# Kernel tuning notes

Measured on AMD Instinct MI355X. Metric: run time of the kernel, lower is better.

Reference implementation:

```python
import jax, jax.numpy as jnp
import numpy as np

W_RAD = 2  # box-filter radius (init kwarg w)
KSIZE = 2 * W_RAD + 1


def _box_conv3d(x, kernel):
    # x: [B,1,D,H,W], kernel: [1,1,k,k,k]; 'same' padding, stride 1
    return jax.lax.conv_general_dilated(
        x, kernel,
        window_strides=(1, 1, 1),
        padding=[(W_RAD, W_RAD)] * 3,
        dimension_numbers=("NCDHW", "OIDHW", "NCDHW"),
    )


def setup_inputs() -> dict:
    key = jax.random.key(0)
    k1, k2 = jax.random.split(key)
    shape = (2, 1, 160, 160, 160)
    M = jax.random.uniform(k1, shape, dtype=jnp.float32)
    R = jax.random.uniform(k2, shape, dtype=jnp.float32)
    kernel = jnp.ones((1, 1, KSIZE, KSIZE, KSIZE), dtype=jnp.float32) / (KSIZE ** 3)
    return {"M": M, "R": R, "kernel": kernel}


def reference(M, R, kernel):
    M_m = _box_conv3d(M, kernel)
    R_m = _box_conv3d(R, kernel)
    MM_m = _box_conv3d(M * M, kernel)
    RR_m = _box_conv3d(R * R, kernel)
    MR_m = _box_conv3d(M * R, kernel)
    M_var = jnp.sqrt(MM_m - M_m ** 2 + 1e-05)
    R_var = jnp.sqrt(RR_m - R_m ** 2 + 1e-05)
    corr = (MR_m - M_m * R_m) / (M_var * R_var + 1e-05)
    return -jnp.mean(corr)
```

## Files before the change

kernel.cpp:

```cpp
#include <hip/hip_runtime.h>
#include <math.h>

#define Bsz 2
#define Dd 160
#define Hh 160
#define Ww 160
#define TH 16
#define TW 32
#define DCHUNK 20
#define NCH 5
#define NT 512
#define HALO_H (TH + 4)
#define HALO_W (TW + 4)
#define APIX (HALO_H * HALO_W)
#define BPIX (HALO_H * TW)
#define NSLICE (DCHUNK + 5)

__global__ void lncc_zero(float* out) { out[0] = 0.0f; }

__global__ __launch_bounds__(NT)
void lncc_main(const float* __restrict__ M,
               const float* __restrict__ R,
               const float* __restrict__ kern,
               float* __restrict__ out)
{
    __shared__ float lm[HALO_H][HALO_W + 1];
    __shared__ float lr[HALO_H][HALO_W + 1];
    __shared__ float sw[NCH][HALO_H][TW + 1];
    __shared__ float red[NT / 64];

    const int tid = threadIdx.x;
    const int tx  = tid & 31;
    const int ty  = tid >> 5;

    const int w0 = blockIdx.x * TW;
    const int h0 = blockIdx.y * TH;
    const int b  = blockIdx.z >> 3;
    const int d0 = (blockIdx.z & 7) * DCHUNK;

    const float k0 = kern[0];

    int  g_off[2], l_off[2];
    bool g_ok[2], l_act[2];
#pragma unroll
    for (int p = 0; p < 2; ++p) {
        int i = tid + p * NT;
        bool act = (i < APIX);
        int yy = act ? (i / HALO_W) : 0;
        int xx = act ? (i - yy * HALO_W) : 0;
        int gh = h0 + yy - 2;
        int gw = w0 + xx - 2;
        l_act[p] = act;
        g_ok[p]  = act && gh >= 0 && gh < Hh && gw >= 0 && gw < Ww;
        g_off[p] = gh * Ww + gw;
        l_off[p] = yy * (HALO_W + 1) + xx;
    }
    float* lmf = &lm[0][0];
    float* lrf = &lr[0][0];

    const size_t batch_base = (size_t)b * Dd * Hh * Ww;

    float pm[2], pr[2];
    auto issue = [&](int s) {
        int  dd  = d0 - 2 + s;
        bool dok = (dd >= 0) && (dd < Dd);
        const float* Mp = M + batch_base + (size_t)(dok ? dd : 0) * (Hh * Ww);
        const float* Rp = R + batch_base + (size_t)(dok ? dd : 0) * (Hh * Ww);
#pragma unroll
        for (int p = 0; p < 2; ++p) {
            bool ok = dok && g_ok[p];
            pm[p] = ok ? Mp[g_off[p]] : 0.0f;
            pr[p] = ok ? Rp[g_off[p]] : 0.0f;
        }
    };

    float ring[5][NCH];
#pragma unroll
    for (int t = 0; t < 5; ++t)
#pragma unroll
        for (int c = 0; c < NCH; ++c) ring[t][c] = 0.0f;

    float acc = 0.0f;

    issue(0);

    for (int s5 = 0; s5 < NSLICE; s5 += 5) {
#pragma unroll
        for (int so = 0; so < 5; ++so) {
            const int s = s5 + so;

#pragma unroll
            for (int p = 0; p < 2; ++p) {
                if (l_act[p]) {
                    lmf[l_off[p]] = pm[p];
                    lrf[l_off[p]] = pr[p];
                }
            }
            __syncthreads();

            if (s + 1 < NSLICE) issue(s + 1);

#pragma unroll
            for (int p = 0; p < 2; ++p) {
                int i = tid + p * NT;
                if (i < BPIX) {
                    int yy = i >> 5;
                    int x  = i & 31;
                    float sm = 0.f, sr = 0.f, smm = 0.f, srr = 0.f, smr = 0.f;
#pragma unroll
                    for (int t = 0; t < 5; ++t) {
                        float a  = lm[yy][x + t];
                        float bb = lr[yy][x + t];
                        sm += a;
                        sr += bb;
                        smm = fmaf(a, a, smm);
                        srr = fmaf(bb, bb, srr);
                        smr = fmaf(a, bb, smr);
                    }
                    sw[0][yy][x] = sm;
                    sw[1][yy][x] = sr;
                    sw[2][yy][x] = smm;
                    sw[3][yy][x] = srr;
                    sw[4][yy][x] = smr;
                }
            }
            __syncthreads();

#pragma unroll
            for (int c = 0; c < NCH; ++c) {
                ring[so][c] = sw[c][ty][tx] + sw[c][ty + 1][tx] + sw[c][ty + 2][tx]
                            + sw[c][ty + 3][tx] + sw[c][ty + 4][tx];
            }

            if (s >= 4 && s < DCHUNK + 4) {
                float S[NCH];
#pragma unroll
                for (int c = 0; c < NCH; ++c)
                    S[c] = ring[0][c] + ring[1][c] + ring[2][c] + ring[3][c] + ring[4][c];
                float Mm  = S[0] * k0;
                float Rm  = S[1] * k0;
                float MMm = S[2] * k0;
                float RRm = S[3] * k0;
                float MRm = S[4] * k0;
                float Mv = sqrtf(MMm - Mm * Mm + 1e-5f);
                float Rv = sqrtf(RRm - Rm * Rm + 1e-5f);
                acc += (MRm - Mm * Rm) / (Mv * Rv + 1e-5f);
            }
        }
    }

#pragma unroll
    for (int off = 32; off > 0; off >>= 1)
        acc += __shfl_down(acc, off, 64);
    if ((tid & 63) == 0) red[tid >> 6] = acc;
    __syncthreads();
    if (tid == 0) {
        float t = 0.f;
#pragma unroll
        for (int i = 0; i < NT / 64; ++i) t += red[i];
        atomicAdd(out, -t * (1.0f / 8192000.0f));
    }
}

extern "C" void kernel_launch(void* const* d_in, const int* in_sizes, int n_in,
                              void* d_out, int out_size, void* d_ws, size_t ws_size,
                              hipStream_t stream) {
    const float* M = (const float*)d_in[0];
    const float* R = (const float*)d_in[1];
    const float* K = (const float*)d_in[2];
    float* out = (float*)d_out;

    lncc_zero<<<1, 1, 0, stream>>>(out);

    dim3 grid(Ww / TW, Hh / TH, Bsz * (Dd / DCHUNK));
    lncc_main<<<grid, NT, 0, stream>>>(M, R, K, out);
}
```

Measured before the change: 143.2 us.

## Prefetch slices two ahead with double buffer and shrink block tiles

```diff
diff --git a/kernel.cpp b/kernel.cpp
--- a/kernel.cpp
+++ b/kernel.cpp
@@ -5,16 +5,17 @@
 #define Dd 160
 #define Hh 160
 #define Ww 160
-#define TH 16
+#define TH 8
 #define TW 32
-#define DCHUNK 20
+#define DCHUNK 16
 #define NCH 5
-#define NT 512
+#define NT 256
 #define HALO_H (TH + 4)
 #define HALO_W (TW + 4)
 #define APIX (HALO_H * HALO_W)
 #define BPIX (HALO_H * TW)
-#define NSLICE (DCHUNK + 5)
+#define NSLICE (DCHUNK + 4)
+#define SLICE_STRIDE (Hh * Ww)
 
 __global__ void lncc_zero(float* out) { out[0] = 0.0f; }
 
@@ -35,8 +36,8 @@
 
     const int w0 = blockIdx.x * TW;
     const int h0 = blockIdx.y * TH;
-    const int b  = blockIdx.z >> 3;
-    const int d0 = (blockIdx.z & 7) * DCHUNK;
+    const int b  = blockIdx.z / 10;
+    const int d0 = (blockIdx.z - b * 10) * DCHUNK;
 
     const float k0 = kern[0];
 
@@ -58,19 +59,19 @@
     float* lmf = &lm[0][0];
     float* lrf = &lr[0][0];
 
-    const size_t batch_base = (size_t)b * Dd * Hh * Ww;
+    const size_t batch_base = (size_t)b * Dd * SLICE_STRIDE;
 
-    float pm[2], pr[2];
-    auto issue = [&](int s) {
+    float pm[2][2], pr[2][2];
+    auto issue = [&](int s, int buf) {
         int  dd  = d0 - 2 + s;
         bool dok = (dd >= 0) && (dd < Dd);
-        const float* Mp = M + batch_base + (size_t)(dok ? dd : 0) * (Hh * Ww);
-        const float* Rp = R + batch_base + (size_t)(dok ? dd : 0) * (Hh * Ww);
+        const float* Mp = M + batch_base + (size_t)(dok ? dd : 0) * SLICE_STRIDE;
+        const float* Rp = R + batch_base + (size_t)(dok ? dd : 0) * SLICE_STRIDE;
 #pragma unroll
         for (int p = 0; p < 2; ++p) {
             bool ok = dok && g_ok[p];
-            pm[p] = ok ? Mp[g_off[p]] : 0.0f;
-            pr[p] = ok ? Rp[g_off[p]] : 0.0f;
+            pm[buf][p] = ok ? Mp[g_off[p]] : 0.0f;
+            pr[buf][p] = ok ? Rp[g_off[p]] : 0.0f;
         }
     };
 
@@ -82,23 +83,26 @@
 
     float acc = 0.0f;
 
-    issue(0);
+    issue(0, 0);
+    issue(1, 1);
 
-    for (int s5 = 0; s5 < NSLICE; s5 += 5) {
+    for (int s10 = 0; s10 < NSLICE; s10 += 10) {
 #pragma unroll
-        for (int so = 0; so < 5; ++so) {
-            const int s = s5 + so;
+        for (int so = 0; so < 10; ++so) {
+            const int s    = s10 + so;
+            const int buf  = so & 1;
+            const int slot = so % 5;
 
 #pragma unroll
             for (int p = 0; p < 2; ++p) {
                 if (l_act[p]) {
-                    lmf[l_off[p]] = pm[p];
-                    lrf[l_off[p]] = pr[p];
+                    lmf[l_off[p]] = pm[buf][p];
+                    lrf[l_off[p]] = pr[buf][p];
                 }
             }
             __syncthreads();
 
-            if (s + 1 < NSLICE) issue(s + 1);
+            if (s + 2 < NSLICE) issue(s + 2, buf);
 
 #pragma unroll
             for (int p = 0; p < 2; ++p) {
@@ -128,11 +132,11 @@
 
 #pragma unroll
             for (int c = 0; c < NCH; ++c) {
-                ring[so][c] = sw[c][ty][tx] + sw[c][ty + 1][tx] + sw[c][ty + 2][tx]
-                            + sw[c][ty + 3][tx] + sw[c][ty + 4][tx];
+                ring[slot][c] = sw[c][ty][tx] + sw[c][ty + 1][tx] + sw[c][ty + 2][tx]
+                              + sw[c][ty + 3][tx] + sw[c][ty + 4][tx];
             }
 
-            if (s >= 4 && s < DCHUNK + 4) {
+            if (s >= 4) {
                 float S[NCH];
 #pragma unroll
                 for (int c = 0; c < NCH; ++c)
```

Result: no change. 142.0 us (-0.9%).

## Restructure box filter with float4 register loads, sliding sums, transposed LDS tile

Applied to the files above, without the earlier changes.

```diff
diff --git a/kernel.cpp b/kernel.cpp
--- a/kernel.cpp
+++ b/kernel.cpp
@@ -5,18 +5,23 @@
 #define Dd 160
 #define Hh 160
 #define Ww 160
-#define TH 16
 #define TW 32
-#define DCHUNK 20
+#define TH 32
+#define DCHUNK 16
+#define NT 320
 #define NCH 5
-#define NT 512
-#define HALO_H (TH + 4)
-#define HALO_W (TW + 4)
-#define APIX (HALO_H * HALO_W)
-#define BPIX (HALO_H * TW)
-#define NSLICE (DCHUNK + 5)
+#define PDIM 48
+#define HROWS (TH + 4)
+#define NSLICE (DCHUNK + 4)
+#define SLICE (Hh * Ww)
 
 __global__ void lncc_zero(float* out) { out[0] = 0.0f; }
+
+__device__ __forceinline__ void bar_lgkm() {
+    asm volatile("s_waitcnt lgkmcnt(0)" ::: "memory");
+    __builtin_amdgcn_s_barrier();
+    asm volatile("" ::: "memory");
+}
 
 __global__ __launch_bounds__(NT)
 void lncc_main(const float* __restrict__ M,
@@ -24,64 +29,63 @@
                const float* __restrict__ kern,
                float* __restrict__ out)
 {
-    __shared__ float lm[HALO_H][HALO_W + 1];
-    __shared__ float lr[HALO_H][HALO_W + 1];
-    __shared__ float sw[NCH][HALO_H][TW + 1];
+    __shared__ float sw[NCH][TW][PDIM];
     __shared__ float red[NT / 64];
 
     const int tid = threadIdx.x;
-    const int tx  = tid & 31;
-    const int ty  = tid >> 5;
-
     const int w0 = blockIdx.x * TW;
     const int h0 = blockIdx.y * TH;
-    const int b  = blockIdx.z >> 3;
-    const int d0 = (blockIdx.z & 7) * DCHUNK;
+    const int b  = blockIdx.z / (Dd / DCHUNK);
+    const int d0 = (blockIdx.z % (Dd / DCHUNK)) * DCHUNK;
 
     const float k0 = kern[0];
 
-    int  g_off[2], l_off[2];
-    bool g_ok[2], l_act[2];
+    const bool isB = tid < HROWS * 8;
+    const int  g   = tid & 7;
+    const int  row = tid >> 3;
+    const int  gh  = h0 + row - 2;
+    const bool hok = isB && gh >= 0 && gh < Hh;
+    bool qok[3]; int qoff[3];
 #pragma unroll
-    for (int p = 0; p < 2; ++p) {
-        int i = tid + p * NT;
-        bool act = (i < APIX);
-        int yy = act ? (i / HALO_W) : 0;
-        int xx = act ? (i - yy * HALO_W) : 0;
-        int gh = h0 + yy - 2;
-        int gw = w0 + xx - 2;
-        l_act[p] = act;
-        g_ok[p]  = act && gh >= 0 && gh < Hh && gw >= 0 && gw < Ww;
-        g_off[p] = gh * Ww + gw;
-        l_off[p] = yy * (HALO_W + 1) + xx;
+    for (int k = 0; k < 3; ++k) {
+        int gw = w0 - 4 + 4 * (g + k);
+        qok[k]  = hok && gw >= 0 && gw <= (Ww - 4);
+        qoff[k] = gh * Ww + gw;
     }
-    float* lmf = &lm[0][0];
-    float* lrf = &lr[0][0];
+    const size_t bbase = (size_t)b * Dd * SLICE;
+    const float* Mb = M + bbase;
+    const float* Rb = R + bbase;
 
-    const size_t batch_base = (size_t)b * Dd * Hh * Ww;
-
-    float pm[2], pr[2];
+    float4 cm[3], cr[3];
     auto issue = [&](int s) {
-        int  dd  = d0 - 2 + s;
-        bool dok = (dd >= 0) && (dd < Dd);
-        const float* Mp = M + batch_base + (size_t)(dok ? dd : 0) * (Hh * Ww);
-        const float* Rp = R + batch_base + (size_t)(dok ? dd : 0) * (Hh * Ww);
+        int dd = d0 - 2 + s;
+        bool dok = dd >= 0 && dd < Dd;
+        const float* Ms = Mb + (size_t)(dok ? dd : 0) * SLICE;
+        const float* Rs = Rb + (size_t)(dok ? dd : 0) * SLICE;
 #pragma unroll
-        for (int p = 0; p < 2; ++p) {
-            bool ok = dok && g_ok[p];
-            pm[p] = ok ? Mp[g_off[p]] : 0.0f;
-            pr[p] = ok ? Rp[g_off[p]] : 0.0f;
+        for (int k = 0; k < 3; ++k) {
+            bool ok = dok && qok[k];
+            cm[k] = ok ? *(const float4*)(Ms + qoff[k]) : make_float4(0.f, 0.f, 0.f, 0.f);
+            cr[k] = ok ? *(const float4*)(Rs + qoff[k]) : make_float4(0.f, 0.f, 0.f, 0.f);
         }
     };
+    float* swp = &sw[0][g * 4][row + 4 * (g & 3)];
 
-    float ring[5][NCH];
+    const bool isC = tid < 256;
+    const int  cw  = tid & 31;
+    const int  hg  = (tid >> 5) & 7;
+    const int  p0  = hg * 4 + 4 * ((cw >> 2) & 3);
+    const float* crd = &sw[0][cw][p0];
+
+    float ring[5][NCH][4];
 #pragma unroll
     for (int t = 0; t < 5; ++t)
 #pragma unroll
-        for (int c = 0; c < NCH; ++c) ring[t][c] = 0.0f;
+        for (int c = 0; c < NCH; ++c)
+#pragma unroll
+            for (int j = 0; j < 4; ++j) ring[t][c][j] = 0.f;
 
-    float acc = 0.0f;
-
+    float acc = 0.f;
     issue(0);
 
     for (int s5 = 0; s5 < NSLICE; s5 += 5) {
@@ -89,75 +93,87 @@
         for (int so = 0; so < 5; ++so) {
             const int s = s5 + so;
 
+            bar_lgkm();
+
+            if (isB) {
+                float am[12], ar[12];
+                *(float4*)&am[0] = cm[0]; *(float4*)&am[4] = cm[1]; *(float4*)&am[8] = cm[2];
+                *(float4*)&ar[0] = cr[0]; *(float4*)&ar[4] = cr[1]; *(float4*)&ar[8] = cr[2];
+                float mm[8], rr[8], mr[8];
 #pragma unroll
-            for (int p = 0; p < 2; ++p) {
-                if (l_act[p]) {
-                    lmf[l_off[p]] = pm[p];
-                    lrf[l_off[p]] = pr[p];
+                for (int k = 0; k < 8; ++k) {
+                    float a = am[k + 2], r_ = ar[k + 2];
+                    mm[k] = a * a; rr[k] = r_ * r_; mr[k] = a * r_;
                 }
-            }
-            __syncthreads();
-
-            if (s + 1 < NSLICE) issue(s + 1);
-
+                float sm  = am[2] + am[3] + am[4] + am[5] + am[6];
+                float sr_ = ar[2] + ar[3] + ar[4] + ar[5] + ar[6];
+                float smm = mm[0] + mm[1] + mm[2] + mm[3] + mm[4];
+                float srr = rr[0] + rr[1] + rr[2] + rr[3] + rr[4];
+                float smr = mr[0] + mr[1] + mr[2] + mr[3] + mr[4];
 #pragma unroll
-            for (int p = 0; p < 2; ++p) {
-                int i = tid + p * NT;
-                if (i < BPIX) {
-                    int yy = i >> 5;
-                    int x  = i & 31;
-                    float sm = 0.f, sr = 0.f, smm = 0.f, srr = 0.f, smr = 0.f;
-#pragma unroll
-                    for (int t = 0; t < 5; ++t) {
-                        float a  = lm[yy][x + t];
-                        float bb = lr[yy][x + t];
-                        sm += a;
-                        sr += bb;
-                        smm = fmaf(a, a, smm);
-                        srr = fmaf(bb, bb, srr);
-                        smr = fmaf(a, bb, smr);
+                for (int j = 0; j < 4; ++j) {
+                    if (j) {
+                        sm  += am[j + 6] - am[j + 1];
+                        sr_ += ar[j + 6] - ar[j + 1];
+                        smm += mm[j + 4] - mm[j - 1];
+                        srr += rr[j + 4] - rr[j - 1];
+                        smr += mr[j + 4] - mr[j - 1];
                     }
-                    sw[0][yy][x] = sm;
-                    sw[1][yy][x] = sr;
-                    sw[2][yy][x] = smm;
-                    sw[3][yy][x] = srr;
-                    sw[4][yy][x] = smr;
+                    float* wp = swp + j * PDIM;
+                    wp[0 * TW * PDIM] = sm;
+                    wp[1 * TW * PDIM] = sr_;
+                    wp[2 * TW * PDIM] = smm;
+                    wp[3 * TW * PDIM] = srr;
+                    wp[4 * TW * PDIM] = smr;
                 }
-            }
-            __syncthreads();
-
-#pragma unroll
-            for (int c = 0; c < NCH; ++c) {
-                ring[so][c] = sw[c][ty][tx] + sw[c][ty + 1][tx] + sw[c][ty + 2][tx]
-                            + sw[c][ty + 3][tx] + sw[c][ty + 4][tx];
+                if (s + 1 < NSLICE) issue(s + 1);
             }
 
-            if (s >= 4 && s < DCHUNK + 4) {
-                float S[NCH];
+            bar_lgkm();
+
+            if (isC) {
+                float hs[NCH][4];
 #pragma unroll
-                for (int c = 0; c < NCH; ++c)
-                    S[c] = ring[0][c] + ring[1][c] + ring[2][c] + ring[3][c] + ring[4][c];
-                float Mm  = S[0] * k0;
-                float Rm  = S[1] * k0;
-                float MMm = S[2] * k0;
-                float RRm = S[3] * k0;
-                float MRm = S[4] * k0;
-                float Mv = sqrtf(MMm - Mm * Mm + 1e-5f);
-                float Rv = sqrtf(RRm - Rm * Rm + 1e-5f);
-                acc += (MRm - Mm * Rm) / (Mv * Rv + 1e-5f);
+                for (int c = 0; c < NCH; ++c) {
+                    float4 A  = *(const float4*)(crd + c * TW * PDIM);
+                    float4 Bq = *(const float4*)(crd + c * TW * PDIM + 4);
+                    float v0 = A.x, v1 = A.y, v2 = A.z, v3 = A.w;
+                    float v4 = Bq.x, v5 = Bq.y, v6 = Bq.z, v7 = Bq.w;
+                    hs[c][0] = v0 + v1 + v2 + v3 + v4;
+                    hs[c][1] = hs[c][0] + v5 - v0;
+                    hs[c][2] = hs[c][1] + v6 - v1;
+                    hs[c][3] = hs[c][2] + v7 - v2;
+#pragma unroll
+                    for (int j = 0; j < 4; ++j) ring[so][c][j] = hs[c][j];
+                }
+                if (s >= 4) {
+#pragma unroll
+                    for (int j = 0; j < 4; ++j) {
+                        float S[NCH];
+#pragma unroll
+                        for (int c = 0; c < NCH; ++c)
+                            S[c] = ring[0][c][j] + ring[1][c][j] + ring[2][c][j]
+                                 + ring[3][c][j] + ring[4][c][j];
+                        float Mm  = S[0] * k0;
+                        float Rm  = S[1] * k0;
+                        float MMm = S[2] * k0;
+                        float RRm = S[3] * k0;
+                        float MRm = S[4] * k0;
+                        float Mv = sqrtf(MMm - Mm * Mm + 1e-5f);
+                        float Rv = sqrtf(RRm - Rm * Rm + 1e-5f);
+                        acc += (MRm - Mm * Rm) / (Mv * Rv + 1e-5f);
+                    }
+                }
             }
         }
     }
 
 #pragma unroll
-    for (int off = 32; off > 0; off >>= 1)
-        acc += __shfl_down(acc, off, 64);
+    for (int off = 32; off; off >>= 1) acc += __shfl_down(acc, off, 64);
     if ((tid & 63) == 0) red[tid >> 6] = acc;
     __syncthreads();
     if (tid == 0) {
-        float t = 0.f;
-#pragma unroll
-        for (int i = 0; i < NT / 64; ++i) t += red[i];
+        float t = red[0] + red[1] + red[2] + red[3] + red[4];
         atomicAdd(out, -t * (1.0f / 8192000.0f));
     }
 }
```

Result: faster. 136.2 us (-4.9%).
